# Kernel tuning notes

Measured on AMD Instinct MI355X. Metric: run time of the kernel, lower is better.

The kernel has to match this reference:

```python
import jax, jax.numpy as jnp
import numpy as np

B, L, D, H = 4, 1024, 256, 8
TEMP = float(np.sqrt(D))
EPS_SM = 1e-6
EPS_LN = 1e-5


def setup_inputs() -> dict:
    key = jax.random.key(0)
    ks = jax.random.split(key, 8)
    std = float(np.sqrt(2.0 / (D * 2)))
    return {
        "q": jax.random.normal(ks[0], (B, L, D), jnp.float32),
        "mask": jax.random.randint(ks[1], (B, L, L), 0, 2, jnp.int32),
        "k": jax.random.normal(ks[2], (B, L, D), jnp.float32),
        "v": jax.random.normal(ks[3], (B, L, D), jnp.float32),
        "w_qs": jax.random.normal(ks[4], (H * D, D), jnp.float32) * std,
        "w_ks": jax.random.normal(ks[5], (H * D, D), jnp.float32) * std,
        "w_vs": jax.random.normal(ks[6], (H * D, D), jnp.float32) * std,
        "fc_w": jax.random.normal(ks[7], (D, H * D), jnp.float32) * float(np.sqrt(2.0 / (D + H * D))),
        "fc_b": jnp.zeros((D,), jnp.float32),
        "ln_g": jnp.ones((D,), jnp.float32),
        "ln_b": jnp.zeros((D,), jnp.float32),
    }


def masked_softmax(x, m):
    # repo's layers.masked_softmax: clamp, mask-mul, stable exp, mask-mul, normalize
    x = jnp.clip(x, -15.0, 15.0) * m
    e = jnp.exp(x - jnp.max(x, axis=-1, keepdims=True)) * m
    return e / (jnp.sum(e, axis=-1, keepdims=True) + EPS_SM)


def reference(q, mask, k, v, w_qs, w_ks, w_vs, fc_w, fc_b, ln_g, ln_b):
    residual = q
    m = mask.astype(q.dtype)[:, None, :, :]          # [B,1,Lq,Lk]
    # projections to per-head full-dim: [B,L,H,D]
    qh = (q @ w_qs.T).reshape(B, L, H, D)
    kh = (k @ w_ks.T).reshape(B, L, H, D)
    vh = (v @ w_vs.T).reshape(B, L, H, D)
    scores = jnp.einsum("bqhd,bkhd->bhqk", qh, kh) / TEMP   # [B,H,Lq,Lk]
    attn = masked_softmax(scores, m)
    out = jnp.einsum("bhqk,bkhd->bqhd", attn, vh).reshape(B, L, H * D)
    out = out @ fc_w.T + fc_b                         # [B,L,D]
    out = out + residual
    mu = jnp.mean(out, axis=-1, keepdims=True)
    var = jnp.var(out, axis=-1, keepdims=True)
    out = (out - mu) / jnp.sqrt(var + EPS_LN) * ln_g + ln_b
    # match torch attn layout: [H*B, Lq, Lk] (head-major)
    attn_hb = jnp.transpose(attn, (1, 0, 2, 3)).reshape(H * B, L, L)
    return out, attn_hb
```

## Files before the change

kernel.cpp:

```cpp
#include <hip/hip_runtime.h>
#include <cstdint>
#include <math.h>

#define Bsz 4
#define Lsz 1024
#define Dsz 256
#define Hsz 8
#define HD  2048
#define NROWS (Bsz*Lsz)
#define INV_TEMP 0.0625f

typedef __attribute__((ext_vector_type(8))) short bf16x8;
typedef __attribute__((ext_vector_type(4))) float f32x4;

__device__ inline unsigned short f2bf(float f) {
    union { float f; unsigned u; } x; x.f = f;
    unsigned r = x.u + 0x7fffu + ((x.u >> 16) & 1u);
    return (unsigned short)(r >> 16);
}
__device__ inline float bf2f(unsigned short u) {
    union { unsigned u; float f; } x; x.u = (unsigned)u << 16; return x.f;
}

#define GBL(p) ((const __attribute__((address_space(1))) unsigned int*)(p))
#define LDS(p) ((__attribute__((address_space(3))) unsigned int*)(p))

template <typename OutT, int EPI>
__global__ __launch_bounds__(256) void gemm_bt(
    const unsigned short* __restrict__ A, const unsigned short* __restrict__ Bm,
    OutT* __restrict__ C,
    int K, int lda, int ldb, int ldc, int inner,
    long long sA1, long long sA2, long long sB1, long long sB2,
    long long sC1, long long sC2, float alpha,
    const int* __restrict__ mask, long long sM2,
    const float* __restrict__ invs, long long sI1, long long sI2)
{
    const int z  = blockIdx.z;
    const int i1 = z / inner;
    const int i2 = z % inner;
    A  += (size_t)i1 * sA1 + (size_t)i2 * sA2;
    Bm += (size_t)i1 * sB1 + (size_t)i2 * sB2;
    C  += (size_t)i1 * sC1 + (size_t)i2 * sC2;
    if (EPI == 1) mask += (size_t)i2 * sM2;
    if (EPI == 2) invs += (size_t)i1 * sI1 + (size_t)i2 * sI2;

    __shared__ unsigned short As[128 * 64];
    __shared__ unsigned short Bs[128 * 64];

    const int t    = threadIdx.x;
    const int lane = t & 63;
    const int w    = t >> 6;
    const int wm   = w & 1;
    const int wn   = w >> 1;
    const int m0   = blockIdx.x * 128;
    const int n0   = blockIdx.y * 128;

    const int rr  = t >> 3;
    const int gch = (((t & 7) ^ (rr & 7))) * 8;
    const unsigned short* gA = A  + (size_t)(m0 + rr) * lda + gch;
    const unsigned short* gB = Bm + (size_t)(n0 + rr) * ldb + gch;
    unsigned short* lA = As + t * 8;
    unsigned short* lB = Bs + t * 8;

    const int fr = lane & 15;
    const int q  = lane >> 4;

    f32x4 acc[4][4];
#pragma unroll
    for (int i = 0; i < 4; ++i)
#pragma unroll
        for (int j = 0; j < 4; ++j) acc[i][j] = (f32x4){0.f, 0.f, 0.f, 0.f};

    for (int k0 = 0; k0 < K; k0 += 64) {
#pragma unroll
        for (int p = 0; p < 4; ++p) {
            __builtin_amdgcn_global_load_lds(GBL(gA + (size_t)p * 32 * lda + k0), LDS(lA + p * 2048), 16, 0, 0);
            __builtin_amdgcn_global_load_lds(GBL(gB + (size_t)p * 32 * ldb + k0), LDS(lB + p * 2048), 16, 0, 0);
        }
        __syncthreads();

#pragma unroll
        for (int s = 0; s < 2; ++s) {
            const int slot = ((s * 4 + q) ^ (fr & 7)) * 8;
            bf16x8 a[4], b[4];
#pragma unroll
            for (int i = 0; i < 4; ++i) a[i] = *(const bf16x8*)(As + (wm * 64 + i * 16 + fr) * 64 + slot);
#pragma unroll
            for (int j = 0; j < 4; ++j) b[j] = *(const bf16x8*)(Bs + (wn * 64 + j * 16 + fr) * 64 + slot);
#pragma unroll
            for (int i = 0; i < 4; ++i)
#pragma unroll
                for (int j = 0; j < 4; ++j)
                    acc[i][j] = __builtin_amdgcn_mfma_f32_16x16x32_bf16(a[i], b[j], acc[i][j], 0, 0, 0);
        }
        __syncthreads();
    }

    const int er = q * 4;
    const int ec = fr;
#pragma unroll
    for (int i = 0; i < 4; ++i) {
        const int mb = m0 + wm * 64 + i * 16 + er;
#pragma unroll
        for (int j = 0; j < 4; ++j) {
            const int n = n0 + wn * 64 + j * 16 + ec;
#pragma unroll
            for (int r = 0; r < 4; ++r) {
                float vv = acc[i][j][r] * alpha;
                if (EPI == 0) {
                    if constexpr (sizeof(OutT) == 4)
                        C[(size_t)(mb + r) * ldc + n] = (OutT)vv;
                    else
                        ((unsigned short*)C)[(size_t)(mb + r) * ldc + n] = f2bf(vv);
                } else if (EPI == 1) {
                    const float m = (float)mask[(size_t)(mb + r) * Lsz + n];
                    vv = fminf(fmaxf(vv, -15.f), 15.f) * m;
                    vv = __expf(vv) * m;
                    ((unsigned short*)C)[(size_t)(mb + r) * ldc + n] = f2bf(vv);
                } else {
                    vv *= invs[mb + r];
                    ((unsigned short*)C)[(size_t)(mb + r) * ldc + n] = f2bf(vv);
                }
            }
        }
    }
}

__global__ __launch_bounds__(256) void cast_all(
    const float* __restrict__ q, const float* __restrict__ k, const float* __restrict__ v,
    const float* __restrict__ wq, const float* __restrict__ wk, const float* __restrict__ wv,
    const float* __restrict__ fw,
    unsigned short* __restrict__ qb, unsigned short* __restrict__ kb, unsigned short* __restrict__ vb,
    unsigned short* __restrict__ wqb, unsigned short* __restrict__ wkb, unsigned short* __restrict__ wvb,
    unsigned short* __restrict__ fwb)
{
    const int gid = blockIdx.x * 256 + threadIdx.x;
    const int NQ = 262144;
    const int NW = 131072;
    const float* src; unsigned short* dst; int off;
    if      (gid < NQ)            { src = q;  dst = qb;  off = gid; }
    else if (gid < 2 * NQ)        { src = k;  dst = kb;  off = gid - NQ; }
    else if (gid < 3 * NQ)        { src = v;  dst = vb;  off = gid - 2 * NQ; }
    else if (gid < 3 * NQ + NW)   { src = wq; dst = wqb; off = gid - 3 * NQ; }
    else if (gid < 3 * NQ + 2*NW) { src = wk; dst = wkb; off = gid - 3 * NQ - NW; }
    else if (gid < 3 * NQ + 3*NW) { src = wv; dst = wvb; off = gid - 3 * NQ - 2 * NW; }
    else                          { src = fw; dst = fwb; off = gid - 3 * NQ - 3 * NW; }
    float4 f = ((const float4*)src)[off];
    ushort4 o;
    o.x = f2bf(f.x); o.y = f2bf(f.y); o.z = f2bf(f.z); o.w = f2bf(f.w);
    ((ushort4*)dst)[off] = o;
}

__global__ __launch_bounds__(256) void norm_kernel(const unsigned short* __restrict__ e,
                                                   float* __restrict__ attn,
                                                   float* __restrict__ invsum)
{
    const int r = blockIdx.x;
    const int t = threadIdx.x;
    const ushort4 u = ((const ushort4*)(e + (size_t)r * Lsz))[t];
    float x0 = bf2f(u.x), x1 = bf2f(u.y), x2 = bf2f(u.z), x3 = bf2f(u.w);
    float s = x0 + x1 + x2 + x3;

    __shared__ float red[4];
#pragma unroll
    for (int o = 32; o > 0; o >>= 1) s += __shfl_down(s, o, 64);
    const int lane = t & 63, w = t >> 6;
    if (lane == 0) red[w] = s;
    __syncthreads();
    const float inv = 1.0f / (red[0] + red[1] + red[2] + red[3] + 1e-6f);

    float4 o4; o4.x = x0 * inv; o4.y = x1 * inv; o4.z = x2 * inv; o4.w = x3 * inv;
    ((float4*)(attn + (size_t)r * Lsz))[t] = o4;
    if (t == 0) invsum[r] = inv;
}

__global__ __launch_bounds__(256) void ln_kernel(const float* __restrict__ gout,
                                                 const float* __restrict__ qin,
                                                 const float* __restrict__ fc_b,
                                                 const float* __restrict__ ln_g,
                                                 const float* __restrict__ ln_b,
                                                 float* __restrict__ out)
{
    const int row = blockIdx.x;
    const int t = threadIdx.x;
    const size_t idx = (size_t)row * Dsz + t;
    const float val = gout[idx] + fc_b[t] + qin[idx];

    __shared__ float red[4];
    float s = val;
#pragma unroll
    for (int o = 32; o > 0; o >>= 1) s += __shfl_down(s, o, 64);
    const int lane = t & 63, w = t >> 6;
    if (lane == 0) red[w] = s;
    __syncthreads();
    const float mu = (red[0] + red[1] + red[2] + red[3]) * (1.0f / Dsz);
    __syncthreads();

    float d = val - mu;
    float s2 = d * d;
#pragma unroll
    for (int o = 32; o > 0; o >>= 1) s2 += __shfl_down(s2, o, 64);
    if (lane == 0) red[w] = s2;
    __syncthreads();
    const float var = (red[0] + red[1] + red[2] + red[3]) * (1.0f / Dsz);

    out[idx] = d * rsqrtf(var + 1e-5f) * ln_g[t] + ln_b[t];
}

extern "C" void kernel_launch(void* const* d_in, const int* in_sizes, int n_in,
                              void* d_out, int out_size, void* d_ws, size_t ws_size,
                              hipStream_t stream)
{
    const float* q    = (const float*)d_in[0];
    const int*   mask = (const int*)d_in[1];
    const float* k    = (const float*)d_in[2];
    const float* v    = (const float*)d_in[3];
    const float* w_qs = (const float*)d_in[4];
    const float* w_ks = (const float*)d_in[5];
    const float* w_vs = (const float*)d_in[6];
    const float* fc_w = (const float*)d_in[7];
    const float* fc_b = (const float*)d_in[8];
    const float* ln_g = (const float*)d_in[9];
    const float* ln_b = (const float*)d_in[10];

    float* out  = (float*)d_out;
    float* attn = (float*)d_out + (size_t)NROWS * Dsz;

    unsigned short* wsu = (unsigned short*)d_ws;
    unsigned short* qh     = wsu;
    unsigned short* kh     = qh + (size_t)NROWS * HD;
    unsigned short* q_bf   = kh + (size_t)NROWS * HD;
    unsigned short* k_bf   = q_bf + (size_t)NROWS * Dsz;
    unsigned short* v_bf   = k_bf + (size_t)NROWS * Dsz;
    unsigned short* wq_bf  = v_bf + (size_t)NROWS * Dsz;
    unsigned short* wk_bf  = wq_bf + (size_t)HD * Dsz;
    unsigned short* wv_bf  = wk_bf + (size_t)HD * Dsz;
    unsigned short* vt     = wv_bf + (size_t)HD * Dsz;
    unsigned short* attn_e = vt + (size_t)Bsz * HD * Lsz;
    unsigned short* attnv  = attn_e + (size_t)32 * Lsz * Lsz;
    unsigned short* fcw_bf = attnv + (size_t)NROWS * HD;
    float*          invsum = (float*)(fcw_bf + (size_t)Dsz * HD);
    float*          fcout  = invsum + 32768;

    dim3 blk(256);

    cast_all<<<dim3(5120), blk, 0, stream>>>(q, k, v, w_qs, w_ks, w_vs, fc_w,
                                             q_bf, k_bf, v_bf, wq_bf, wk_bf, wv_bf, fcw_bf);

    {
        dim3 grid(NROWS / 128, HD / 128, 2);
        gemm_bt<unsigned short, 0><<<grid, blk, 0, stream>>>(q_bf, wq_bf, qh,
            Dsz, Dsz, Dsz, HD, 2,
            0, (long long)NROWS * Dsz, 0, (long long)HD * Dsz, 0, (long long)NROWS * HD,
            1.0f, nullptr, 0, nullptr, 0, 0);
    }

    {
        dim3 grid(HD / 128, Lsz / 128, Bsz);
        gemm_bt<unsigned short, 0><<<grid, blk, 0, stream>>>(wv_bf, v_bf, vt,
            Dsz, Dsz, Dsz, Lsz, 1,
            0, 0, (long long)Lsz * Dsz, 0, (long long)HD * Lsz, 0,
            1.0f, nullptr, 0, nullptr, 0, 0);
    }

    {
        dim3 grid(Lsz / 128, Lsz / 128, Hsz * Bsz);
        gemm_bt<unsigned short, 1><<<grid, blk, 0, stream>>>(qh, kh, attn_e,
            Dsz, HD, HD, Lsz, Bsz,
            Dsz, (long long)Lsz * HD, Dsz, (long long)Lsz * HD,
            (long long)Bsz * Lsz * Lsz, (long long)Lsz * Lsz,
            INV_TEMP, mask, (long long)Lsz * Lsz, nullptr, 0, 0);
    }

    norm_kernel<<<dim3(32 * Lsz), blk, 0, stream>>>(attn_e, attn, invsum);

    {
        dim3 grid(Lsz / 128, Dsz / 128, Hsz * Bsz);
        gemm_bt<unsigned short, 2><<<grid, blk, 0, stream>>>(attn_e, vt, attnv,
            Lsz, Lsz, Lsz, HD, Bsz,
            (long long)Bsz * Lsz * Lsz, (long long)Lsz * Lsz,
            (long long)Dsz * Lsz, (long long)HD * Lsz,
            Dsz, (long long)Lsz * HD,
            1.0f, nullptr, 0, invsum, (long long)Bsz * Lsz, (long long)Lsz);
    }

    {
        dim3 grid(NROWS / 128, Dsz / 128, 1);
        gemm_bt<float, 0><<<grid, blk, 0, stream>>>(attnv, fcw_bf, fcout,
            HD, HD, HD, Dsz, 1, 0, 0, 0, 0, 0, 0,
            1.0f, nullptr, 0, nullptr, 0, 0);
    }

    ln_kernel<<<dim3(NROWS), blk, 0, stream>>>(fcout, q, fc_b, ln_g, ln_b, out);
}
```

Before: 362.2 us.

## Template GEMM tile sizes, split-K the output projection, warp-per-row softmax normalize

Turns the bf16 MFMA GEMM into a template over tile shape and occupancy hint, and picks per-GEMM tiles (64x256 or 128x256). The output projection becomes a 4-way split-K whose partial sums are added in the layernorm kernel. The normalize kernel now handles one row per wavefront with shuffle-xor reductions and no LDS sync. The aim is to raise occupancy and parallelism on narrow GEMMs and cut per-block overhead, at the cost of extra fp32 partial traffic and larger per-block register tiles.

```diff
diff --git a/kernel.cpp b/kernel.cpp
--- a/kernel.cpp
+++ b/kernel.cpp
@@ -25,8 +25,8 @@
 #define GBL(p) ((const __attribute__((address_space(1))) unsigned int*)(p))
 #define LDS(p) ((__attribute__((address_space(3))) unsigned int*)(p))
 
-template <typename OutT, int EPI>
-__global__ __launch_bounds__(256) void gemm_bt(
+template <int TMv, int TNv, typename OutT, int EPI, int MINW>
+__global__ __launch_bounds__(256, MINW) void gemm_bt(
     const unsigned short* __restrict__ A, const unsigned short* __restrict__ Bm,
     OutT* __restrict__ C,
     int K, int lda, int ldb, int ldc, int inner,
@@ -35,6 +35,10 @@
     const int* __restrict__ mask, long long sM2,
     const float* __restrict__ invs, long long sI1, long long sI2)
 {
+    constexpr int WMv = TMv / 2, WNv = TNv / 2;
+    constexpr int IT = TMv / 32, JT = TNv / 32;
+    constexpr int APASS = TMv / 32, NPASS = (TMv + TNv) / 32;
+
     const int z  = blockIdx.z;
     const int i1 = z / inner;
     const int i2 = z % inner;
@@ -44,82 +48,83 @@
     if (EPI == 1) mask += (size_t)i2 * sM2;
     if (EPI == 2) invs += (size_t)i1 * sI1 + (size_t)i2 * sI2;
 
-    __shared__ unsigned short As[128 * 64];
-    __shared__ unsigned short Bs[128 * 64];
+    __shared__ unsigned short S[(TMv + TNv) * 64];
+    unsigned short* As = S;
+    unsigned short* Bs = S + TMv * 64;
 
     const int t    = threadIdx.x;
     const int lane = t & 63;
     const int w    = t >> 6;
     const int wm   = w & 1;
     const int wn   = w >> 1;
-    const int m0   = blockIdx.x * 128;
-    const int n0   = blockIdx.y * 128;
-
-    const int rr  = t >> 3;
-    const int gch = (((t & 7) ^ (rr & 7))) * 8;
-    const unsigned short* gA = A  + (size_t)(m0 + rr) * lda + gch;
-    const unsigned short* gB = Bm + (size_t)(n0 + rr) * ldb + gch;
-    unsigned short* lA = As + t * 8;
-    unsigned short* lB = Bs + t * 8;
+    const int m0   = blockIdx.x * TMv;
+    const int n0   = blockIdx.y * TNv;
+
+    const int rA = t >> 3;
+    const int ch = (((t & 7) ^ (rA & 7))) * 8;
+    const unsigned short* gA = A  + (size_t)(m0 + rA) * lda + ch;
+    const unsigned short* gB = Bm + (size_t)(n0 + rA) * ldb + ch;
 
     const int fr = lane & 15;
     const int q  = lane >> 4;
 
-    f32x4 acc[4][4];
-#pragma unroll
-    for (int i = 0; i < 4; ++i)
-#pragma unroll
-        for (int j = 0; j < 4; ++j) acc[i][j] = (f32x4){0.f, 0.f, 0.f, 0.f};
+    f32x4 acc[IT][JT];
+#pragma unroll
+    for (int i = 0; i < IT; ++i)
+#pragma unroll
+        for (int j = 0; j < JT; ++j) acc[i][j] = (f32x4){0.f, 0.f, 0.f, 0.f};
 
     for (int k0 = 0; k0 < K; k0 += 64) {
 #pragma unroll
-        for (int p = 0; p < 4; ++p) {
-            __builtin_amdgcn_global_load_lds(GBL(gA + (size_t)p * 32 * lda + k0), LDS(lA + p * 2048), 16, 0, 0);
-            __builtin_amdgcn_global_load_lds(GBL(gB + (size_t)p * 32 * ldb + k0), LDS(lB + p * 2048), 16, 0, 0);
+        for (int p = 0; p < NPASS; ++p) {
+            const unsigned short* src = (p < APASS)
+                ? (gA + (size_t)p * 32 * lda + k0)
+                : (gB + (size_t)(p - APASS) * 32 * ldb + k0);
+            __builtin_amdgcn_global_load_lds(GBL(src), LDS(S + p * 2048 + t * 8), 16, 0, 0);
         }
         __syncthreads();
 
 #pragma unroll
-        for (int s = 0; s < 2; ++s) {
-            const int slot = ((s * 4 + q) ^ (fr & 7)) * 8;
-            bf16x8 a[4], b[4];
-#pragma unroll
-            for (int i = 0; i < 4; ++i) a[i] = *(const bf16x8*)(As + (wm * 64 + i * 16 + fr) * 64 + slot);
-#pragma unroll
-            for (int j = 0; j < 4; ++j) b[j] = *(const bf16x8*)(Bs + (wn * 64 + j * 16 + fr) * 64 + slot);
-#pragma unroll
-            for (int i = 0; i < 4; ++i)
-#pragma unroll
-                for (int j = 0; j < 4; ++j)
+        for (int ks = 0; ks < 2; ++ks) {
+            const int slot = ((ks * 4 + q) ^ (fr & 7)) * 8;
+            bf16x8 a[IT], b[JT];
+#pragma unroll
+            for (int i = 0; i < IT; ++i)
+                a[i] = *(const bf16x8*)(As + (wm * WMv + i * 16 + fr) * 64 + slot);
+#pragma unroll
+            for (int j = 0; j < JT; ++j)
+                b[j] = *(const bf16x8*)(Bs + (wn * WNv + j * 16 + fr) * 64 + slot);
+#pragma unroll
+            for (int i = 0; i < IT; ++i)
+#pragma unroll
+                for (int j = 0; j < JT; ++j)
                     acc[i][j] = __builtin_amdgcn_mfma_f32_16x16x32_bf16(a[i], b[j], acc[i][j], 0, 0, 0);
         }
         __syncthreads();
     }
 
-    const int er = q * 4;
-    const int ec = fr;
-#pragma unroll
-    for (int i = 0; i < 4; ++i) {
-        const int mb = m0 + wm * 64 + i * 16 + er;
-#pragma unroll
-        for (int j = 0; j < 4; ++j) {
-            const int n = n0 + wn * 64 + j * 16 + ec;
-#pragma unroll
-            for (int r = 0; r < 4; ++r) {
+#pragma unroll
+    for (int i = 0; i < IT; ++i) {
+#pragma unroll
+        for (int r = 0; r < 4; ++r) {
+            const int row = m0 + wm * WMv + i * 16 + q * 4 + r;
+#pragma unroll
+            for (int j = 0; j < JT; ++j) {
+                const int col = n0 + wn * WNv + j * 16 + fr;
                 float vv = acc[i][j][r] * alpha;
                 if (EPI == 0) {
                     if constexpr (sizeof(OutT) == 4)
-                        C[(size_t)(mb + r) * ldc + n] = (OutT)vv;
+                        C[(size_t)row * ldc + col] = (OutT)vv;
                     else
-                        ((unsigned short*)C)[(size_t)(mb + r) * ldc + n] = f2bf(vv);
+                        ((unsigned short*)C)[(size_t)row * ldc + col] = f2bf(vv);
                 } else if (EPI == 1) {
-                    const float m = (float)mask[(size_t)(mb + r) * Lsz + n];
+                    const float m = (float)mask[(size_t)row * Lsz + col];
                     vv = fminf(fmaxf(vv, -15.f), 15.f) * m;
                     vv = __expf(vv) * m;
-                    ((unsigned short*)C)[(size_t)(mb + r) * ldc + n] = f2bf(vv);
+                    ((unsigned short*)C)[(size_t)row * ldc + col] = f2bf(vv);
                 } else {
-                    vv *= invs[mb + r];
-                    ((unsigned short*)C)[(size_t)(mb + r) * ldc + n] = f2bf(vv);
+                    vv *= invs[row];
+                    ((unsigned short*)C)[(size_t)row * ldc + col] = f2bf(vv);
                 }
             }
         }
@@ -155,23 +160,31 @@
                                                    float* __restrict__ attn,
                                                    float* __restrict__ invsum)
 {
-    const int r = blockIdx.x;
-    const int t = threadIdx.x;
-    const ushort4 u = ((const ushort4*)(e + (size_t)r * Lsz))[t];
-    float x0 = bf2f(u.x), x1 = bf2f(u.y), x2 = bf2f(u.z), x3 = bf2f(u.w);
-    float s = x0 + x1 + x2 + x3;
-
-    __shared__ float red[4];
-#pragma unroll
-    for (int o = 32; o > 0; o >>= 1) s += __shfl_down(s, o, 64);
-    const int lane = t & 63, w = t >> 6;
-    if (lane == 0) red[w] = s;
-    __syncthreads();
-    const float inv = 1.0f / (red[0] + red[1] + red[2] + red[3] + 1e-6f);
-
-    float4 o4; o4.x = x0 * inv; o4.y = x1 * inv; o4.z = x2 * inv; o4.w = x3 * inv;
-    ((float4*)(attn + (size_t)r * Lsz))[t] = o4;
-    if (t == 0) invsum[r] = inv;
+    const int r    = blockIdx.x * 4 + (threadIdx.x >> 6);
+    const int lane = threadIdx.x & 63;
+    const unsigned short* rowp = e + (size_t)r * Lsz + lane * 16;
+
+    union { uint4 v[2]; unsigned short u[16]; } buf;
+    buf.v[0] = *(const uint4*)rowp;
+    buf.v[1] = *(const uint4*)(rowp + 8);
+
+    float f[16];
+    float s = 0.f;
+#pragma unroll
+    for (int i = 0; i < 16; ++i) { f[i] = bf2f(buf.u[i]); s += f[i]; }
+#pragma unroll
+    for (int o = 1; o <= 32; o <<= 1) s += __shfl_xor(s, o, 64);
+    const float inv = 1.0f / (s + 1e-6f);
+
+    float* op = attn + (size_t)r * Lsz + lane * 16;
+#pragma unroll
+    for (int c = 0; c < 4; ++c) {
+        float4 o4;
+        o4.x = f[c * 4 + 0] * inv; o4.y = f[c * 4 + 1] * inv;
+        o4.z = f[c * 4 + 2] * inv; o4.w = f[c * 4 + 3] * inv;
+        *(float4*)(op + c * 4) = o4;
+    }
+    if (lane == 0) invsum[r] = inv;
 }
 
 __global__ __launch_bounds__(256) void ln_kernel(const float* __restrict__ gout,
@@ -184,7 +197,9 @@
     const int row = blockIdx.x;
     const int t = threadIdx.x;
     const size_t idx = (size_t)row * Dsz + t;
-    const float val = gout[idx] + fc_b[t] + qin[idx];
+    const size_t P = (size_t)NROWS * Dsz;
+    const float val = gout[idx] + gout[idx + P] + gout[idx + 2 * P] + gout[idx + 3 * P]
+                    + fc_b[t] + qin[idx];
 
     __shared__ float red[4];
     float s = val;
@@ -248,35 +263,35 @@
                                              q_bf, k_bf, v_bf, wq_bf, wk_bf, wv_bf, fcw_bf);
 
     {
-        dim3 grid(NROWS / 128, HD / 128, 2);
-        gemm_bt<unsigned short, 0><<<grid, blk, 0, stream>>>(q_bf, wq_bf, qh,
+        dim3 grid(NROWS / 64, HD / 256, 2);
+        gemm_bt<64, 256, unsigned short, 0, 3><<<grid, blk, 0, stream>>>(q_bf, wq_bf, qh,
             Dsz, Dsz, Dsz, HD, 2,
             0, (long long)NROWS * Dsz, 0, (long long)HD * Dsz, 0, (long long)NROWS * HD,
             1.0f, nullptr, 0, nullptr, 0, 0);
     }
 
     {
-        dim3 grid(HD / 128, Lsz / 128, Bsz);
-        gemm_bt<unsigned short, 0><<<grid, blk, 0, stream>>>(wv_bf, v_bf, vt,
+        dim3 grid(HD / 64, Lsz / 256, Bsz);
+        gemm_bt<64, 256, unsigned short, 0, 3><<<grid, blk, 0, stream>>>(wv_bf, v_bf, vt,
             Dsz, Dsz, Dsz, Lsz, 1,
             0, 0, (long long)Lsz * Dsz, 0, (long long)HD * Lsz, 0,
             1.0f, nullptr, 0, nullptr, 0, 0);
     }
 
     {
-        dim3 grid(Lsz / 128, Lsz / 128, Hsz * Bsz);
-        gemm_bt<unsigned short, 1><<<grid, blk, 0, stream>>>(qh, kh, attn_e,
+        dim3 grid(Lsz / 128, Lsz / 256, Hsz * Bsz);
+        gemm_bt<128, 256, unsigned short, 1, 2><<<grid, blk, 0, stream>>>(qh, kh, attn_e,
             Dsz, HD, HD, Lsz, Bsz,
             Dsz, (long long)Lsz * HD, Dsz, (long long)Lsz * HD,
             (long long)Bsz * Lsz * Lsz, (long long)Lsz * Lsz,
             INV_TEMP, mask, (long long)Lsz * Lsz, nullptr, 0, 0);
     }
 
-    norm_kernel<<<dim3(32 * Lsz), blk, 0, stream>>>(attn_e, attn, invsum);
-
-    {
-        dim3 grid(Lsz / 128, Dsz / 128, Hsz * Bsz);
-        gemm_bt<unsigned short, 2><<<grid, blk, 0, stream>>>(attn_e, vt, attnv,
+    norm_kernel<<<dim3(32 * Lsz / 4), blk, 0, stream>>>(attn_e, attn, invsum);
+
+    {
+        dim3 grid(Lsz / 64, Dsz / 256, Hsz * Bsz);
+        gemm_bt<64, 256, unsigned short, 2, 3><<<grid, blk, 0, stream>>>(attn_e, vt, attnv,
             Lsz, Lsz, Lsz, HD, Bsz,
             (long long)Bsz * Lsz * Lsz, (long long)Lsz * Lsz,
             (long long)Dsz * Lsz, (long long)HD * Lsz,
@@ -285,9 +300,10 @@
     }
 
     {
-        dim3 grid(NROWS / 128, Dsz / 128, 1);
-        gemm_bt<float, 0><<<grid, blk, 0, stream>>>(attnv, fcw_bf, fcout,
-            HD, HD, HD, Dsz, 1, 0, 0, 0, 0, 0, 0,
+        dim3 grid(NROWS / 64, Dsz / 256, 4);
+        gemm_bt<64, 256, float, 0, 3><<<grid, blk, 0, stream>>>(attnv, fcw_bf, fcout,
+            512, HD, HD, Dsz, 4,
+            0, 512, 0, 512, 0, (long long)NROWS * Dsz,
             1.0f, nullptr, 0, nullptr, 0, 0);
     }
 
```

Result: faster. 348.2 us (-3.9%).
